# Kernel optimization log

Hardware: AMD Instinct MI355X
Metric: run time of the kernel (lower is better)

## Reference

```python
import jax, jax.numpy as jnp
import numpy as np

N_OBS = 2_097_152
N_BAND = 4
T_SPAN = 3650.0  # days


def setup_inputs() -> dict:
    key = jax.random.key(0)
    k0, k1, k2, k3, k4, k5 = jax.random.split(key, 6)
    t = jnp.sort(jax.random.uniform(k0, (N_OBS,), jnp.float32) * T_SPAN)
    band = jax.random.randint(k1, (N_OBS,), 0, N_BAND)
    y = jax.random.normal(k2, (N_OBS,), jnp.float32)
    yerr = 0.1 + 0.9 * jax.random.uniform(k3, (N_OBS,), jnp.float32)
    log_amp_delta = 0.1 * jax.random.normal(k4, (N_BAND - 1,), jnp.float32)
    # [log sigma, log ell] for the quasisep Exp kernel
    log_kernel_param = jnp.array([0.0, np.log(50.0)], dtype=jnp.float32) + \
        0.1 * jax.random.normal(k5, (2,), jnp.float32)
    return {"t": t, "band": band, "y": y, "yerr": yerr,
            "log_amp_delta": log_amp_delta, "log_kernel_param": log_kernel_param}


def _log_prob(t, band, y, yerr, log_amp_delta, log_kernel_param):
    # amp_transform: prepend 0 -> per-band amplitudes
    amps = jnp.exp(jnp.concatenate([jnp.zeros(1, log_amp_delta.dtype), log_amp_delta]))
    sigma2 = jnp.exp(2.0 * log_kernel_param[0])
    ell = jnp.exp(log_kernel_param[1])

    # lag_transform with zero lags: sort by time (assume_sorted path of tinygp)
    inds = jnp.argsort(t)
    ts, b = t[inds], band[inds]
    ys, dg = y[inds], (yerr ** 2)[inds]

    # multiband Exp kernel: K_ij = sigma2 * u_i * u_j * exp(-(t_i - t_j)/ell), i>=j
    u = amps[b]                       # per-point amplitude
    a = dg + sigma2 * u * u           # diagonal K_ii + noise
    U = sigma2 * u                    # semiseparable left factor
    V = u                             # semiseparable right factor
    dt = jnp.diff(ts)
    P = jnp.concatenate([jnp.zeros(1, ts.dtype), jnp.exp(-dt / ell)])  # decay factors

    # Celerite O(N) Cholesky (K = L D L^T) fused with the forward solve L z = y.
    def step(carry, x):
        cS, cg = carry                # cS = S_{n-1} + D_{n-1} W_{n-1}^2 ; cg = g_{n-1} + W_{n-1} z_{n-1}
        Pn, an, Un, Vn, yn = x
        Sn = Pn * Pn * cS
        gn = Pn * cg
        Dn = an - Un * Un * Sn
        Wn = (Vn - Sn * Un) / Dn
        zn = yn - Un * gn
        return (Sn + Dn * Wn * Wn, gn + Wn * zn), (jnp.log(Dn), zn * zn / Dn)

    zero = jnp.zeros((), ts.dtype)
    _, (logD, quad) = jax.lax.scan(step, (zero, zero), (P, a, U, V, ys))
    n = ts.shape[0]
    return -0.5 * (jnp.sum(quad) + jnp.sum(logD) + n * jnp.log(2.0 * jnp.pi))


def reference(t, band, y, yerr, log_amp_delta, log_kernel_param):
    return _log_prob(t, band, y, yerr, log_amp_delta, log_kernel_param)
```

## Files before the change

kernel.cpp:

```cpp
#include <hip/hip_runtime.h>
#include <math.h>

#define N_TOTAL 2097152
#define NT 256
#define NC 16
#define EPB (NT * NC)
#define NB (N_TOTAL / EPB)
#define NTH (NB * NT)

struct DMat { double al, be, ga, de, c, e, f; };

__device__ __forceinline__ DMat dmat_identity() {
    DMat m; m.al = 1.0; m.be = 0.0; m.ga = 0.0; m.de = 1.0; m.c = 1.0; m.e = 0.0; m.f = 0.0;
    return m;
}

__device__ __forceinline__ DMat dmat_compose(const DMat& A, const DMat& B) {
    DMat r;
    r.al = A.al * B.al + A.be * B.ga;
    r.be = A.al * B.be + A.be * B.de;
    r.ga = A.ga * B.al + A.de * B.ga;
    r.de = A.ga * B.be + A.de * B.de;
    r.c  = A.c * B.c;
    r.e  = A.e * B.al + A.c * B.e + A.f * B.ga;
    r.f  = A.e * B.be + A.c * B.f + A.f * B.de;
    return r;
}

__device__ __forceinline__ void dmat_normalize(DMat& m) {
    double mx = fmax(fabs(m.al), fabs(m.be));
    mx = fmax(mx, fabs(m.ga));
    mx = fmax(mx, fabs(m.de));
    mx = fmax(mx, fabs(m.c));
    mx = fmax(mx, fabs(m.e));
    mx = fmax(mx, fabs(m.f));
    if (!(mx > 0.0) || isinf(mx)) return;
    double inv = 1.0 / mx;
    m.al *= inv; m.be *= inv; m.ga *= inv; m.de *= inv;
    m.c *= inv; m.e *= inv; m.f *= inv;
}

__device__ __forceinline__ void dmat_store(double* sm, int i, const DMat& m) {
    sm[0 * NT + i] = m.al; sm[1 * NT + i] = m.be; sm[2 * NT + i] = m.ga;
    sm[3 * NT + i] = m.de; sm[4 * NT + i] = m.c;  sm[5 * NT + i] = m.e;
    sm[6 * NT + i] = m.f;
}

__device__ __forceinline__ DMat dmat_load(const double* sm, int i) {
    DMat m;
    m.al = sm[0 * NT + i]; m.be = sm[1 * NT + i]; m.ga = sm[2 * NT + i];
    m.de = sm[3 * NT + i]; m.c  = sm[4 * NT + i]; m.e  = sm[5 * NT + i];
    m.f  = sm[6 * NT + i];
    return m;
}

__device__ __forceinline__ DMat dmat_scan_inclusive(double* sm, DMat mine, int tid) {
    dmat_store(sm, tid, mine);
    __syncthreads();
    for (int d = 1; d < NT; d <<= 1) {
        DMat o;
        bool has = (tid >= d);
        if (has) o = dmat_load(sm, tid - d);
        __syncthreads();
        if (has) {
            mine = dmat_compose(mine, o);
            dmat_normalize(mine);
            dmat_store(sm, tid, mine);
        }
        __syncthreads();
    }
    return mine;
}

__device__ __forceinline__ DMat elem_mat(double P, double a, double U, double V, double yy) {
    double p = P * P;
    DMat m;
    m.al = p * (a - 2.0 * U * V);
    m.be = V * V;
    m.ga = -(p * U * U);
    m.de = a;
    m.c  = P * (a - U * V);
    m.e  = -(yy * p * U);
    m.f  = yy * V;
    return m;
}

__device__ __forceinline__ double band_amp(int b, double a1, double a2, double a3) {
    double lo = (b & 1) ? a1 : 1.0;
    double hi = (b & 1) ? a3 : a2;
    return (b & 2) ? hi : lo;
}

__global__ __launch_bounds__(NT) void k_upsweep(
    const float* __restrict__ t, const int* __restrict__ band,
    const float* __restrict__ y, const float* __restrict__ yerr,
    const float* __restrict__ lad, const float* __restrict__ lkp,
    double* __restrict__ ptc)
{
    __shared__ double sm[7 * NT];
    const int tid = threadIdx.x;
    const double sigma2 = exp(2.0 * (double)lkp[0]);
    const float inv_ell_f = expf(-lkp[1]);
    const double amp1 = exp((double)lad[0]);
    const double amp2 = exp((double)lad[1]);
    const double amp3 = exp((double)lad[2]);

    const int gid = blockIdx.x * NT + tid;
    const int base = gid * NC;
    const bool first = (base == 0);

    float tpA = first ? 0.0f : t[base - 1];
    float tpB = t[base + NC / 2 - 1];

    DMat accA = dmat_identity();
    DMat accB = dmat_identity();

    #pragma unroll
    for (int kk = 0; kk < NC / 2; kk += 4) {
        float4 tvA = *reinterpret_cast<const float4*>(t + base + kk);
        float4 yvA = *reinterpret_cast<const float4*>(y + base + kk);
        float4 evA = *reinterpret_cast<const float4*>(yerr + base + kk);
        int4   bvA = *reinterpret_cast<const int4*>(band + base + kk);
        float4 tvB = *reinterpret_cast<const float4*>(t + base + NC / 2 + kk);
        float4 yvB = *reinterpret_cast<const float4*>(y + base + NC / 2 + kk);
        float4 evB = *reinterpret_cast<const float4*>(yerr + base + NC / 2 + kk);
        int4   bvB = *reinterpret_cast<const int4*>(band + base + NC / 2 + kk);
        float tA[4] = {tvA.x, tvA.y, tvA.z, tvA.w};
        float yA[4] = {yvA.x, yvA.y, yvA.z, yvA.w};
        float eA[4] = {evA.x, evA.y, evA.z, evA.w};
        int   bA[4] = {bvA.x, bvA.y, bvA.z, bvA.w};
        float tB[4] = {tvB.x, tvB.y, tvB.z, tvB.w};
        float yB[4] = {yvB.x, yvB.y, yvB.z, yvB.w};
        float eB[4] = {evB.x, evB.y, evB.z, evB.w};
        int   bB[4] = {bvB.x, bvB.y, bvB.z, bvB.w};
        #pragma unroll
        for (int j = 0; j < 4; ++j) {
            {
                double u = band_amp(bA[j], amp1, amp2, amp3);
                double U = sigma2 * u;
                double a = (double)eA[j] * (double)eA[j] + U * u;
                float dt = tA[j] - tpA; tpA = tA[j];
                double P = (first && kk == 0 && j == 0)
                         ? 0.0 : (double)expf(-dt * inv_ell_f);
                accA = dmat_compose(elem_mat(P, a, U, u, (double)yA[j]), accA);
            }
            {
                double u = band_amp(bB[j], amp1, amp2, amp3);
                double U = sigma2 * u;
                double a = (double)eB[j] * (double)eB[j] + U * u;
                float dt = tB[j] - tpB; tpB = tB[j];
                double P = (double)expf(-dt * inv_ell_f);
                accB = dmat_compose(elem_mat(P, a, U, u, (double)yB[j]), accB);
            }
        }
    }
    DMat acc = dmat_compose(accB, accA);
    dmat_normalize(acc);
    DMat incl = dmat_scan_inclusive(sm, acc, tid);
    ptc[0 * NTH + gid] = incl.al; ptc[1 * NTH + gid] = incl.be;
    ptc[2 * NTH + gid] = incl.ga; ptc[3 * NTH + gid] = incl.de;
    ptc[4 * NTH + gid] = incl.c;  ptc[5 * NTH + gid] = incl.e;
    ptc[6 * NTH + gid] = incl.f;
}

__global__ __launch_bounds__(NT) void k_spine(
    const double* __restrict__ ptc, double* __restrict__ block_excl,
    double* __restrict__ accum, unsigned int* __restrict__ done)
{
    __shared__ double sm[7 * NT];
    const int tid = threadIdx.x;
    if (tid == 0) { accum[0] = 0.0; accum[1] = 0.0; *done = 0u; }
    const int g0 = (2 * tid) * NT + (NT - 1);
    const int g1 = (2 * tid + 1) * NT + (NT - 1);
    DMat m0 = {ptc[0 * NTH + g0], ptc[1 * NTH + g0], ptc[2 * NTH + g0],
               ptc[3 * NTH + g0], ptc[4 * NTH + g0], ptc[5 * NTH + g0],
               ptc[6 * NTH + g0]};
    DMat m1 = {ptc[0 * NTH + g1], ptc[1 * NTH + g1], ptc[2 * NTH + g1],
               ptc[3 * NTH + g1], ptc[4 * NTH + g1], ptc[5 * NTH + g1],
               ptc[6 * NTH + g1]};
    DMat mine = dmat_compose(m1, m0);
    dmat_normalize(mine);
    dmat_scan_inclusive(sm, mine, tid);
    DMat E = (tid == 0) ? dmat_identity() : dmat_load(sm, tid - 1);
    double* o0 = block_excl + (2 * tid) * 7;
    o0[0] = E.al; o0[1] = E.be; o0[2] = E.ga; o0[3] = E.de;
    o0[4] = E.c;  o0[5] = E.e;  o0[6] = E.f;
    DMat M = dmat_compose(m0, E);
    dmat_normalize(M);
    double* o1 = block_excl + (2 * tid + 1) * 7;
    o1[0] = M.al; o1[1] = M.be; o1[2] = M.ga; o1[3] = M.de;
    o1[4] = M.c;  o1[5] = M.e;  o1[6] = M.f;
}

__global__ __launch_bounds__(NT) void k_replay(
    const float* __restrict__ t, const int* __restrict__ band,
    const float* __restrict__ y, const float* __restrict__ yerr,
    const float* __restrict__ lad, const float* __restrict__ lkp,
    const double* __restrict__ ptc, const double* __restrict__ block_excl,
    double* __restrict__ accum, unsigned int* __restrict__ done,
    float* __restrict__ out)
{
    const int tid = threadIdx.x;
    const int gid = blockIdx.x * NT + tid;
    const double sigma2 = exp(2.0 * (double)lkp[0]);
    const float inv_ell_f = expf(-lkp[1]);
    const double amp1 = exp((double)lad[0]);
    const double amp2 = exp((double)lad[1]);
    const double amp3 = exp((double)lad[2]);

    const double* pb = block_excl + blockIdx.x * 7;
    DMat Eb = {pb[0], pb[1], pb[2], pb[3], pb[4], pb[5], pb[6]};
    DMat F;
    if (tid == 0) {
        F = Eb;
    } else {
        const int gm1 = gid - 1;
        DMat E = {ptc[0 * NTH + gm1], ptc[1 * NTH + gm1], ptc[2 * NTH + gm1],
                  ptc[3 * NTH + gm1], ptc[4 * NTH + gm1], ptc[5 * NTH + gm1],
                  ptc[6 * NTH + gm1]};
        F = dmat_compose(E, Eb);
    }
    dmat_normalize(F);
    double x = 0.0, g = 0.0;
    if (F.de != 0.0 && !isinf(F.de)) {
        double invde = 1.0 / F.de;
        x = F.be * invde;
        g = F.f  * invde;
    }
    if (!isfinite(x)) x = 0.0;
    if (!isfinite(g)) g = 0.0;

    const int base = gid * NC;
    const bool first = (base == 0);
    float tp = first ? 0.0f : t[base - 1];

    double s_logD = 0.0, s_quad = 0.0, pd = 1.0;
    #pragma unroll
    for (int k = 0; k < NC; k += 4) {
        float4 tv = *reinterpret_cast<const float4*>(t + base + k);
        float4 yv = *reinterpret_cast<const float4*>(y + base + k);
        float4 ev = *reinterpret_cast<const float4*>(yerr + base + k);
        int4   bv = *reinterpret_cast<const int4*>(band + base + k);
        float tc[4] = {tv.x, tv.y, tv.z, tv.w};
        float yc[4] = {yv.x, yv.y, yv.z, yv.w};
        float ec[4] = {ev.x, ev.y, ev.z, ev.w};
        int   bc[4] = {bv.x, bv.y, bv.z, bv.w};
        #pragma unroll
        for (int j = 0; j < 4; ++j) {
            double u = band_amp(bc[j], amp1, amp2, amp3);
            double U = sigma2 * u;
            double a = (double)ec[j] * (double)ec[j] + U * u;
            float dt = tc[j] - tp; tp = tc[j];
            double P = (first && k == 0 && j == 0)
                     ? 0.0 : (double)expf(-dt * inv_ell_f);
            double p = P * P;
            double S = p * x;
            double D = a - U * U * S;
            if (!(D > 1e-300)) D = 1e-300;
            double invD = 1.0 / D;
            double W = (u - S * U) * invD;
            double gn = P * g;
            double z = (double)yc[j] - U * gn;
            pd *= D;
            s_quad = fma(z * z, invD, s_quad);
            x = fma(D * W, W, S);
            g = fma(W, z, gn);
        }
        if (((k + 4) & 7) == 0) {
            s_logD += log(pd);
            pd = 1.0;
        }
    }

    #pragma unroll
    for (int off = 32; off > 0; off >>= 1) {
        s_logD += __shfl_down(s_logD, off);
        s_quad += __shfl_down(s_quad, off);
    }
    __shared__ double red[8];
    const int wid = tid >> 6, lane = tid & 63;
    if (lane == 0) { red[wid] = s_logD; red[4 + wid] = s_quad; }
    __syncthreads();
    if (tid == 0) {
        double l = red[0] + red[1] + red[2] + red[3];
        double q = red[4] + red[5] + red[6] + red[7];
        atomicAdd(&accum[0], l);
        atomicAdd(&accum[1], q);
        __threadfence();
        unsigned int old = atomicAdd(done, 1u);
        if (old == NB - 1) {
            double L = atomicAdd(&accum[0], 0.0);
            double Q = atomicAdd(&accum[1], 0.0);
            out[0] = (float)(-0.5 * (Q + L
                     + (double)N_TOTAL * 1.8378770664093454836));
        }
    }
}

extern "C" void kernel_launch(void* const* d_in, const int* in_sizes, int n_in,
                              void* d_out, int out_size, void* d_ws, size_t ws_size,
                              hipStream_t stream)
{
    const float* t    = (const float*)d_in[0];
    const int*   band = (const int*)d_in[1];
    const float* y    = (const float*)d_in[2];
    const float* yerr = (const float*)d_in[3];
    const float* lad  = (const float*)d_in[4];
    const float* lkp  = (const float*)d_in[5];

    double* dws        = (double*)d_ws;
    double* ptc        = dws;
    double* block_excl = dws + 7 * NTH;
    double* accum      = dws + 7 * NTH + 7 * NB;
    unsigned int* done = (unsigned int*)(dws + 7 * NTH + 7 * NB + 2);

    k_upsweep<<<NB, NT, 0, stream>>>(t, band, y, yerr, lad, lkp, ptc);
    k_spine<<<1, NT, 0, stream>>>(ptc, block_excl, accum, done);
    k_replay<<<NB, NT, 0, stream>>>(t, band, y, yerr, lad, lkp,
                                    ptc, block_excl, accum, done, (float*)d_out);
}
```

Baseline: 128.4 us.

## Fuse upsweep, spine and replay into one persistent kernel with grid barrier

```diff
diff --git a/kernel.cpp b/kernel.cpp
--- a/kernel.cpp
+++ b/kernel.cpp
@@ -2,11 +2,10 @@
 #include <math.h>
 
 #define N_TOTAL 2097152
-#define NT 256
+#define NT 512
 #define NC 16
 #define EPB (NT * NC)
 #define NB (N_TOTAL / EPB)
-#define NTH (NB * NT)
 
 struct DMat { double al, be, ga, de, c, e, f; };
 
@@ -72,6 +71,21 @@
     return mine;
 }
 
+__device__ __forceinline__ void dmat_scan_spine(double* sm, int tid) {
+    for (int d = 1; d < NB; d <<= 1) {
+        DMat mine, o;
+        bool has = (tid >= d) && (tid < NB);
+        if (has) { mine = dmat_load(sm, tid); o = dmat_load(sm, tid - d); }
+        __syncthreads();
+        if (has) {
+            mine = dmat_compose(mine, o);
+            dmat_normalize(mine);
+            dmat_store(sm, tid, mine);
+        }
+        __syncthreads();
+    }
+}
+
 __device__ __forceinline__ DMat elem_mat(double P, double a, double U, double V, double yy) {
     double p = P * P;
     DMat m;
@@ -91,23 +105,30 @@
     return (b & 2) ? hi : lo;
 }
 
-__global__ __launch_bounds__(NT) void k_upsweep(
+__global__ __launch_bounds__(NT) void k_fused(
     const float* __restrict__ t, const int* __restrict__ band,
     const float* __restrict__ y, const float* __restrict__ yerr,
     const float* __restrict__ lad, const float* __restrict__ lkp,
-    double* __restrict__ ptc)
+    double* __restrict__ L, double* __restrict__ accum,
+    unsigned int* __restrict__ bar0, unsigned int* __restrict__ done,
+    float* __restrict__ out)
 {
     __shared__ double sm[7 * NT];
+    __shared__ double red[16];
     const int tid = threadIdx.x;
+    const int bid = blockIdx.x;
+
     const double sigma2 = exp(2.0 * (double)lkp[0]);
     const float inv_ell_f = expf(-lkp[1]);
     const double amp1 = exp((double)lad[0]);
     const double amp2 = exp((double)lad[1]);
     const double amp3 = exp((double)lad[2]);
 
-    const int gid = blockIdx.x * NT + tid;
+    const int gid = bid * NT + tid;
     const int base = gid * NC;
     const bool first = (base == 0);
+
+    float Pv[NC], av[NC], Uv[NC], Vv[NC], yvv[NC];
 
     float tpA = first ? 0.0f : t[base - 1];
     float tpB = t[base + NC / 2 - 1];
@@ -140,86 +161,61 @@
                 double U = sigma2 * u;
                 double a = (double)eA[j] * (double)eA[j] + U * u;
                 float dt = tA[j] - tpA; tpA = tA[j];
-                double P = (first && kk == 0 && j == 0)
-                         ? 0.0 : (double)expf(-dt * inv_ell_f);
-                accA = dmat_compose(elem_mat(P, a, U, u, (double)yA[j]), accA);
+                float pf = (first && kk == 0 && j == 0)
+                         ? 0.0f : expf(-dt * inv_ell_f);
+                Pv[kk + j] = pf; av[kk + j] = (float)a;
+                Uv[kk + j] = (float)U; Vv[kk + j] = (float)u;
+                yvv[kk + j] = yA[j];
+                accA = dmat_compose(elem_mat((double)pf, a, U, u, (double)yA[j]), accA);
             }
             {
                 double u = band_amp(bB[j], amp1, amp2, amp3);
                 double U = sigma2 * u;
                 double a = (double)eB[j] * (double)eB[j] + U * u;
                 float dt = tB[j] - tpB; tpB = tB[j];
-                double P = (double)expf(-dt * inv_ell_f);
-                accB = dmat_compose(elem_mat(P, a, U, u, (double)yB[j]), accB);
+                float pf = expf(-dt * inv_ell_f);
+                int ix = 8 + kk + j;
+                Pv[ix] = pf; av[ix] = (float)a;
+                Uv[ix] = (float)U; Vv[ix] = (float)u;
+                yvv[ix] = yB[j];
+                accB = dmat_compose(elem_mat((double)pf, a, U, u, (double)yB[j]), accB);
             }
         }
     }
     DMat acc = dmat_compose(accB, accA);
     dmat_normalize(acc);
     DMat incl = dmat_scan_inclusive(sm, acc, tid);
-    ptc[0 * NTH + gid] = incl.al; ptc[1 * NTH + gid] = incl.be;
-    ptc[2 * NTH + gid] = incl.ga; ptc[3 * NTH + gid] = incl.de;
-    ptc[4 * NTH + gid] = incl.c;  ptc[5 * NTH + gid] = incl.e;
-    ptc[6 * NTH + gid] = incl.f;
-}
-
-__global__ __launch_bounds__(NT) void k_spine(
-    const double* __restrict__ ptc, double* __restrict__ block_excl,
-    double* __restrict__ accum, unsigned int* __restrict__ done)
-{
-    __shared__ double sm[7 * NT];
-    const int tid = threadIdx.x;
-    if (tid == 0) { accum[0] = 0.0; accum[1] = 0.0; *done = 0u; }
-    const int g0 = (2 * tid) * NT + (NT - 1);
-    const int g1 = (2 * tid + 1) * NT + (NT - 1);
-    DMat m0 = {ptc[0 * NTH + g0], ptc[1 * NTH + g0], ptc[2 * NTH + g0],
-               ptc[3 * NTH + g0], ptc[4 * NTH + g0], ptc[5 * NTH + g0],
-               ptc[6 * NTH + g0]};
-    DMat m1 = {ptc[0 * NTH + g1], ptc[1 * NTH + g1], ptc[2 * NTH + g1],
-               ptc[3 * NTH + g1], ptc[4 * NTH + g1], ptc[5 * NTH + g1],
-               ptc[6 * NTH + g1]};
-    DMat mine = dmat_compose(m1, m0);
-    dmat_normalize(mine);
-    dmat_scan_inclusive(sm, mine, tid);
-    DMat E = (tid == 0) ? dmat_identity() : dmat_load(sm, tid - 1);
-    double* o0 = block_excl + (2 * tid) * 7;
-    o0[0] = E.al; o0[1] = E.be; o0[2] = E.ga; o0[3] = E.de;
-    o0[4] = E.c;  o0[5] = E.e;  o0[6] = E.f;
-    DMat M = dmat_compose(m0, E);
-    dmat_normalize(M);
-    double* o1 = block_excl + (2 * tid + 1) * 7;
-    o1[0] = M.al; o1[1] = M.be; o1[2] = M.ga; o1[3] = M.de;
-    o1[4] = M.c;  o1[5] = M.e;  o1[6] = M.f;
-}
-
-__global__ __launch_bounds__(NT) void k_replay(
-    const float* __restrict__ t, const int* __restrict__ band,
-    const float* __restrict__ y, const float* __restrict__ yerr,
-    const float* __restrict__ lad, const float* __restrict__ lkp,
-    const double* __restrict__ ptc, const double* __restrict__ block_excl,
-    double* __restrict__ accum, unsigned int* __restrict__ done,
-    float* __restrict__ out)
-{
-    const int tid = threadIdx.x;
-    const int gid = blockIdx.x * NT + tid;
-    const double sigma2 = exp(2.0 * (double)lkp[0]);
-    const float inv_ell_f = expf(-lkp[1]);
-    const double amp1 = exp((double)lad[0]);
-    const double amp2 = exp((double)lad[1]);
-    const double amp3 = exp((double)lad[2]);
-
-    const double* pb = block_excl + blockIdx.x * 7;
-    DMat Eb = {pb[0], pb[1], pb[2], pb[3], pb[4], pb[5], pb[6]};
-    DMat F;
+
+    DMat Et = (tid == 0) ? dmat_identity() : dmat_load(sm, tid - 1);
+
+    if (tid == NT - 1) {
+        double* o = L + bid * 7;
+        o[0] = incl.al; o[1] = incl.be; o[2] = incl.ga; o[3] = incl.de;
+        o[4] = incl.c;  o[5] = incl.e;  o[6] = incl.f;
+    }
+
+    __syncthreads();
     if (tid == 0) {
-        F = Eb;
-    } else {
-        const int gm1 = gid - 1;
-        DMat E = {ptc[0 * NTH + gm1], ptc[1 * NTH + gm1], ptc[2 * NTH + gm1],
-                  ptc[3 * NTH + gm1], ptc[4 * NTH + gm1], ptc[5 * NTH + gm1],
-                  ptc[6 * NTH + gm1]};
-        F = dmat_compose(E, Eb);
-    }
+        __threadfence();
+        atomicAdd(bar0, 1u);
+        while (__hip_atomic_load(bar0, __ATOMIC_ACQUIRE,
+                                 __HIP_MEMORY_SCOPE_AGENT) < NB) {
+            __builtin_amdgcn_s_sleep(2);
+        }
+    }
+    __syncthreads();
+
+    if (tid < NB) {
+        const double* p = L + tid * 7;
+        DMat m = {p[0], p[1], p[2], p[3], p[4], p[5], p[6]};
+        dmat_store(sm, tid, m);
+    }
+    __syncthreads();
+    dmat_scan_spine(sm, tid);
+    DMat Eb = dmat_identity();
+    if (bid > 0) Eb = dmat_load(sm, bid - 1);
+
+    DMat F = dmat_compose(Et, Eb);
     dmat_normalize(F);
     double x = 0.0, g = 0.0;
     if (F.de != 0.0 && !isinf(F.de)) {
@@ -230,43 +226,24 @@
     if (!isfinite(x)) x = 0.0;
     if (!isfinite(g)) g = 0.0;
 
-    const int base = gid * NC;
-    const bool first = (base == 0);
-    float tp = first ? 0.0f : t[base - 1];
-
     double s_logD = 0.0, s_quad = 0.0, pd = 1.0;
     #pragma unroll
-    for (int k = 0; k < NC; k += 4) {
-        float4 tv = *reinterpret_cast<const float4*>(t + base + k);
-        float4 yv = *reinterpret_cast<const float4*>(y + base + k);
-        float4 ev = *reinterpret_cast<const float4*>(yerr + base + k);
-        int4   bv = *reinterpret_cast<const int4*>(band + base + k);
-        float tc[4] = {tv.x, tv.y, tv.z, tv.w};
-        float yc[4] = {yv.x, yv.y, yv.z, yv.w};
-        float ec[4] = {ev.x, ev.y, ev.z, ev.w};
-        int   bc[4] = {bv.x, bv.y, bv.z, bv.w};
-        #pragma unroll
-        for (int j = 0; j < 4; ++j) {
-            double u = band_amp(bc[j], amp1, amp2, amp3);
-            double U = sigma2 * u;
-            double a = (double)ec[j] * (double)ec[j] + U * u;
-            float dt = tc[j] - tp; tp = tc[j];
-            double P = (first && k == 0 && j == 0)
-                     ? 0.0 : (double)expf(-dt * inv_ell_f);
-            double p = P * P;
-            double S = p * x;
-            double D = a - U * U * S;
-            if (!(D > 1e-300)) D = 1e-300;
-            double invD = 1.0 / D;
-            double W = (u - S * U) * invD;
-            double gn = P * g;
-            double z = (double)yc[j] - U * gn;
-            pd *= D;
-            s_quad = fma(z * z, invD, s_quad);
-            x = fma(D * W, W, S);
-            g = fma(W, z, gn);
-        }
-        if (((k + 4) & 7) == 0) {
+    for (int k = 0; k < NC; ++k) {
+        double P = (double)Pv[k], a = (double)av[k], U = (double)Uv[k];
+        double V = (double)Vv[k], yy = (double)yvv[k];
+        double p = P * P;
+        double S = p * x;
+        double D = a - U * U * S;
+        if (!(D > 1e-300)) D = 1e-300;
+        double invD = 1.0 / D;
+        double W = (V - S * U) * invD;
+        double gn = P * g;
+        double z = yy - U * gn;
+        pd *= D;
+        s_quad = fma(z * z, invD, s_quad);
+        x = fma(D * W, W, S);
+        g = fma(W, z, gn);
+        if ((k & 7) == 7) {
             s_logD += log(pd);
             pd = 1.0;
         }
@@ -277,21 +254,21 @@
         s_logD += __shfl_down(s_logD, off);
         s_quad += __shfl_down(s_quad, off);
     }
-    __shared__ double red[8];
     const int wid = tid >> 6, lane = tid & 63;
-    if (lane == 0) { red[wid] = s_logD; red[4 + wid] = s_quad; }
+    if (lane == 0) { red[wid] = s_logD; red[8 + wid] = s_quad; }
     __syncthreads();
     if (tid == 0) {
-        double l = red[0] + red[1] + red[2] + red[3];
-        double q = red[4] + red[5] + red[6] + red[7];
+        double l = 0.0, q = 0.0;
+        #pragma unroll
+        for (int w = 0; w < 8; ++w) { l += red[w]; q += red[8 + w]; }
         atomicAdd(&accum[0], l);
         atomicAdd(&accum[1], q);
         __threadfence();
         unsigned int old = atomicAdd(done, 1u);
         if (old == NB - 1) {
-            double L = atomicAdd(&accum[0], 0.0);
-            double Q = atomicAdd(&accum[1], 0.0);
-            out[0] = (float)(-0.5 * (Q + L
+            double LL = atomicAdd(&accum[0], 0.0);
+            double QQ = atomicAdd(&accum[1], 0.0);
+            out[0] = (float)(-0.5 * (QQ + LL
                      + (double)N_TOTAL * 1.8378770664093454836));
         }
     }
@@ -309,13 +286,11 @@
     const float* lkp  = (const float*)d_in[5];
 
     double* dws        = (double*)d_ws;
-    double* ptc        = dws;
-    double* block_excl = dws + 7 * NTH;
-    double* accum      = dws + 7 * NTH + 7 * NB;
-    unsigned int* done = (unsigned int*)(dws + 7 * NTH + 7 * NB + 2);
-
-    k_upsweep<<<NB, NT, 0, stream>>>(t, band, y, yerr, lad, lkp, ptc);
-    k_spine<<<1, NT, 0, stream>>>(ptc, block_excl, accum, done);
-    k_replay<<<NB, NT, 0, stream>>>(t, band, y, yerr, lad, lkp,
-                                    ptc, block_excl, accum, done, (float*)d_out);
-}
+    double* accum      = dws;
+    unsigned int* ctrs = (unsigned int*)(dws + 2);
+    double* L          = dws + 4;
+
+    hipMemsetAsync(dws, 0, 32, stream);
+    k_fused<<<NB, NT, 0, stream>>>(t, band, y, yerr, lad, lkp,
+                                   L, accum, ctrs, ctrs + 1, (float*)d_out);
+}
```

Result: faster. 122.6 us (-4.5%).
